# Kernel optimization log

Measured on AMD Instinct MI355X. Metric: run time of the kernel, lower is better.

## Reference

```python
import jax, jax.numpy as jnp
import numpy as np

N = 4096    # nodes per graph
C = 128     # in_channels == out_channels
HEAD = 1
E = 65536   # edges per graph (avg degree 16)


def setup_inputs() -> dict:
    key = jax.random.key(0)
    ks = jax.random.split(key, 24)
    def w(k, shape):
        return jax.random.normal(k, shape, dtype=jnp.float32) * 0.05
    return {
        "x1": jax.random.normal(ks[0], (N, C), dtype=jnp.float32),
        "x2": jax.random.normal(ks[1], (N, C), dtype=jnp.float32),
        "edge_index1": jax.random.randint(ks[2], (2, E), 0, N),
        "edge_index2": jax.random.randint(ks[3], (2, E), 0, N),
        "wl1_w": w(ks[4], (HEAD * C, C)), "wl1_b": w(ks[5], (HEAD * C,)),
        "wr1_w": w(ks[6], (HEAD * C, C)), "wr1_b": w(ks[7], (HEAD * C,)),
        "al1": w(ks[8], (HEAD, C)), "ar1": w(ks[9], (HEAD, C)),
        "wl2_w": w(ks[10], (HEAD * C, C)), "wl2_b": w(ks[11], (HEAD * C,)),
        "wr2_w": w(ks[12], (HEAD * C, C)), "wr2_b": w(ks[13], (HEAD * C,)),
        "al2": w(ks[14], (HEAD, C)), "ar2": w(ks[15], (HEAD, C)),
        "w1_w": w(ks[16], (C, 2 * C)), "w1_b": w(ks[17], (C,)),
        "w2_w": w(ks[18], (C, 2 * C)), "w2_b": w(ks[19], (C,)),
        "lin_w": w(ks[20], (HEAD * C, C)), "lin_b": w(ks[21], (HEAD * C,)),
    }


def _leaky_relu(x):
    return jnp.where(x > 0, x, 0.2 * x)


def _attention(src, tgt, wl, bl, wr, br, al, ar):
    # alpha_l: (N_src,), alpha_r: (N_tot,) -> dense (N_src, N_tot) softmax
    a_l = ((src @ wl.T + bl).reshape(-1, HEAD, C) * al[None]).sum(-1).mean(1)
    a_r = ((tgt @ wr.T + br).reshape(-1, HEAD, C) * ar[None]).sum(-1).mean(1)
    return jax.nn.softmax(_leaky_relu(a_l[:, None] + a_r[None, :]), axis=1)


def _aggr_update(x_i, tgt_all, ei, wl, bl, wr, br, al, ar, ww, wb):
    att = _attention(x_i, tgt_all, wl, bl, wr, br, al, ar)   # (N_i, N_tot)
    ot = x_i - att @ tgt_all                                  # (N_i, C)
    feat = jnp.concatenate([x_i, ot], axis=1)                 # (N_i, 2C)
    n = x_i.shape[0]
    loops = jnp.arange(n)                                     # add_self_loops
    src = jnp.concatenate([ei[0], loops])
    dst = jnp.concatenate([ei[1], loops])
    sums = jax.ops.segment_sum(feat[dst], src, num_segments=n)
    cnt = jax.ops.segment_sum(jnp.ones((src.shape[0],), feat.dtype), src, num_segments=n)
    aggr = sums / cnt[:, None]                                # scatter 'mean'
    return jax.nn.relu(aggr) @ ww.T + wb


def reference(x1, x2, edge_index1, edge_index2,
              wl1_w, wl1_b, wr1_w, wr1_b, al1, ar1,
              wl2_w, wl2_b, wr2_w, wr2_b, al2, ar2,
              w1_w, w1_b, w2_w, w2_b, lin_w, lin_b):
    Xs = [x1, x2]
    eis = [edge_index1, edge_index2]
    layers = [(wl1_w, wl1_b, wr1_w, wr1_b, al1, ar1, w1_w, w1_b),
              (wl2_w, wl2_b, wr2_w, wr2_b, al2, ar2, w2_w, w2_b)]
    for (wl, bl, wr, br, al, ar, ww, wb) in layers:
        tgt = jnp.concatenate(Xs, axis=0)
        Xs = [_aggr_update(Xs[i], tgt, eis[i], wl, bl, wr, br, al, ar, ww, wb)
              for i in range(2)]
    feats = jnp.concatenate(Xs, axis=0) @ lin_w.T + lin_b     # (2N, C)
    return jax.nn.sigmoid(feats @ feats.T)                    # (2N, 2N)
```

## Files before the change

kernel.cpp:

```cpp
#include <hip/hip_runtime.h>
#include <hip/hip_bf16.h>

#define NT 8192
#define NN 4096
#define CD 128
#define NE 65536

typedef __attribute__((ext_vector_type(8))) short bf16x8;
typedef __attribute__((ext_vector_type(16))) float f32x16;
typedef __attribute__((ext_vector_type(4))) float f32x4;

__global__ __launch_bounds__(256) void k_prep(
    const float* __restrict__ x1, const float* __restrict__ x2, float* __restrict__ X,
    const float* __restrict__ W1, const float* __restrict__ W2, const float* __restrict__ WL,
    float* __restrict__ WT1, float* __restrict__ WT2, float* __restrict__ WTL,
    const float* __restrict__ wlw0, const float* __restrict__ wlb0,
    const float* __restrict__ wrw0, const float* __restrict__ wrb0,
    const float* __restrict__ al0, const float* __restrict__ ar0,
    const float* __restrict__ wlw1, const float* __restrict__ wlb1,
    const float* __restrict__ wrw1, const float* __restrict__ wrb1,
    const float* __restrict__ al1, const float* __restrict__ ar1,
    float* __restrict__ VP, int* __restrict__ DEG) {
  int b = blockIdx.x, tid = threadIdx.x;
  int gid = b * 256 + tid;
  {
    const f32x4* s1 = (const f32x4*)x1;
    const f32x4* s2 = (const f32x4*)x2;
    f32x4* d = (f32x4*)X;
    d[gid] = s1[gid];
    d[gid + NN * CD / 4] = s2[gid];
  }
  if (gid < 81920) {
    int idx = gid;
    if (idx < 32768) { int c = idx >> 8, k = idx & 255; WT1[k * 128 + c] = W1[idx]; }
    else if (idx < 65536) { int j = idx - 32768; int c = j >> 8, k = j & 255; WT2[k * 128 + c] = W2[j]; }
    else { int j = idx - 65536; int c = j >> 7, k = j & 127; WTL[k * 128 + c] = WL[j]; }
  }
  if ((b == 508 || b == 509) && tid < 128) {
    int L = b - 508;
    const float* wlw = L ? wlw1 : wlw0;
    const float* wlb = L ? wlb1 : wlb0;
    const float* wrw = L ? wrw1 : wrw0;
    const float* wrb = L ? wrb1 : wrb0;
    const float* alv = L ? al1 : al0;
    const float* arv = L ? ar1 : ar0;
    float* vp = VP + L * 258;
    int c = tid;
    float sl = 0.f, sr = 0.f;
    for (int h = 0; h < 128; ++h) {
      sl += wlw[h * 128 + c] * alv[h];
      sr += wrw[h * 128 + c] * arv[h];
    }
    vp[c] = sl;
    vp[128 + c] = sr;
    if (c < 2) {
      const float* bb = c ? wrb : wlb;
      const float* aa = c ? arv : alv;
      float s = 0.f;
      for (int h = 0; h < 128; ++h) s += bb[h] * aa[h];
      vp[256 + c] = s;
    }
  }
  if (gid < 2 * NN) DEG[gid] = 0;
}

__device__ inline void alar_row(const float* __restrict__ X, const float* __restrict__ VP,
                                float* __restrict__ AL, float* __restrict__ AR,
                                int row, int lane) {
  float x0 = X[row * 128 + lane], x1 = X[row * 128 + 64 + lane];
  float sl = x0 * VP[lane] + x1 * VP[64 + lane];
  float sr = x0 * VP[128 + lane] + x1 * VP[192 + lane];
  #pragma unroll
  for (int m = 1; m < 64; m <<= 1) {
    sl += __shfl_xor(sl, m, 64);
    sr += __shfl_xor(sr, m, 64);
  }
  if (lane == 0) { AL[row] = sl + VP[256]; AR[row] = sr + VP[257]; }
}

__device__ void rank_body(int rb, int tid, const float* __restrict__ AR,
                          int* __restrict__ RANK) {
  __shared__ float tile[1024];
  int jb = rb & 31, tb = rb >> 5;
  int base = tb * 1024;
  for (int t = tid; t < 1024; t += 256) tile[t] = AR[base + t];
  __syncthreads();
  int j = jb * 256 + tid;
  float aj = AR[j];
  int cnt = 0;
  #pragma unroll 8
  for (int u = 0; u < 1024; ++u) {
    float a2 = tile[u];
    cnt += (a2 < aj || (a2 == aj && (base + u) < j)) ? 1 : 0;
  }
  atomicAdd(&RANK[j], cnt);
}

__device__ void scanoff_body(int g, int tid, const int* __restrict__ DEG,
                             int* __restrict__ OFFS, int* __restrict__ CURS) {
  __shared__ int part[256];
  int loc[16];
  int s = 0;
  #pragma unroll
  for (int i = 0; i < 16; ++i) { loc[i] = s; s += DEG[g * NN + tid * 16 + i]; }
  part[tid] = s;
  __syncthreads();
  for (int d = 1; d < 256; d <<= 1) {
    int v = part[tid];
    int o = (tid >= d) ? part[tid - d] : 0;
    __syncthreads();
    part[tid] = v + o;
    __syncthreads();
  }
  int excl = tid ? part[tid - 1] : 0;
  #pragma unroll
  for (int i = 0; i < 16; ++i) {
    int o = excl + loc[i];
    OFFS[g * (NN + 1) + tid * 16 + i] = o;
    CURS[g * NN + tid * 16 + i] = o;
  }
  if (tid == 255) OFFS[g * (NN + 1) + NN] = part[255];
}

__global__ __launch_bounds__(256) void k_s2(
    const int* __restrict__ EI1, const int* __restrict__ EI2, int* __restrict__ DEG,
    const float* __restrict__ X, const float* __restrict__ VP0,
    float* __restrict__ AL, float* __restrict__ AR, int* __restrict__ RANK) {
  int b = blockIdx.x, tid = threadIdx.x;
  if (b < 512) {
    int gid = b * 256 + tid;
    int g = gid >> 16, e = gid & 65535;
    const int* src = g ? EI2 : EI1;
    atomicAdd(&DEG[g * NN + src[e]], 1);
  } else {
    int bb = b - 512;
    if (bb < 32) RANK[bb * 256 + tid] = 0;
    alar_row(X, VP0, AL, AR, bb * 4 + (tid >> 6), tid & 63);
  }
}

__global__ __launch_bounds__(256) void k_s3(
    const int* __restrict__ DEG, int* __restrict__ OFFS, int* __restrict__ CURS,
    const float* __restrict__ AR, int* __restrict__ RANK) {
  int b = blockIdx.x, tid = threadIdx.x;
  if (b < 2) scanoff_body(b, tid, DEG, OFFS, CURS);
  else rank_body(b - 2, tid, AR, RANK);
}

__global__ __launch_bounds__(256) void k_s4(
    const int* __restrict__ EI1, const int* __restrict__ EI2,
    int* __restrict__ CURS, int* __restrict__ ADJ,
    const int* __restrict__ RANK, const float* __restrict__ AR,
    int* __restrict__ PERM, float* __restrict__ ARS) {
  int b = blockIdx.x, tid = threadIdx.x;
  if (b < 512) {
    int gid = b * 256 + tid;
    int g = gid >> 16, e = gid & 65535;
    const int* ei = g ? EI2 : EI1;
    int s = ei[e], d = ei[NE + e];
    int pos = atomicAdd(&CURS[g * NN + s], 1);
    ADJ[g * NE + pos] = d;
  } else {
    int j = (b - 512) * 256 + tid;
    int r = RANK[j];
    PERM[r] = j;
    ARS[r] = AR[j];
  }
}

__global__ void k_rank(const float* __restrict__ AR, int* __restrict__ RANK) {
  rank_body(blockIdx.x, threadIdx.x, AR, RANK);
}
__global__ void k_perm(const int* __restrict__ RANK, const float* __restrict__ AR,
                       int* __restrict__ PERM, float* __restrict__ ARS) {
  int j = blockIdx.x * 256 + threadIdx.x;
  int r = RANK[j];
  PERM[r] = j;
  ARS[r] = AR[j];
}

__global__ __launch_bounds__(256) void k_scanA(
    const float* __restrict__ X, const int* __restrict__ PERM,
    const float* __restrict__ ARS, int* __restrict__ RANK,
    float* __restrict__ P1, float* __restrict__ P2,
    float* __restrict__ CT1, float* __restrict__ CT2,
    float* __restrict__ Q1L, float* __restrict__ Q2L,
    float* __restrict__ QCT1, float* __restrict__ QCT2) {
  __shared__ int pc[64];
  __shared__ float w[2][64];
  __shared__ float part[2][4][32];
  __shared__ float qpart[2][4];
  int b = blockIdx.x;
  if (b < 32) RANK[b * 256 + threadIdx.x] = 0;
  int chunk = b >> 2, sub = b & 3;
  int tid = threadIdx.x;
  int a = tid >> 7;
  int g = (tid >> 5) & 3;
  int cl = tid & 31;
  int c = sub * 32 + cl;
  if (tid < 64) {
    int r = chunk * 64 + tid;
    pc[tid] = PERM[r];
    float ar = ARS[r];
    w[0][tid] = __expf(ar);
    w[1][tid] = __expf(0.2f * ar);
  }
  __syncthreads();
  int t0 = g * 16;
  float loc[16];
  float acc = 0.f;
  #pragma unroll 4
  for (int t = 0; t < 16; ++t) {
    acc += w[a][t0 + t] * X[pc[t0 + t] * 128 + c];
    loc[t] = acc;
  }
  part[a][g][cl] = acc;
  float qloc[16];
  float qacc = 0.f;
  bool doQ = (sub == 0 && cl == 0);
  if (doQ) {
    for (int t = 0; t < 16; ++t) { qacc += w[a][t0 + t]; qloc[t] = qacc; }
    qpart[a][g] = qacc;
  }
  __syncthreads();
  float off = (g > 0 ? part[a][0][cl] : 0.f) + (g > 1 ? part[a][1][cl] : 0.f) +
              (g > 2 ? part[a][2][cl] : 0.f);
  float* P = a ? P2 : P1;
  #pragma unroll 4
  for (int t = 0; t < 16; ++t) P[(chunk * 64 + t0 + t) * 128 + c] = loc[t] + off;
  if (g == 3) (a ? CT2 : CT1)[chunk * 128 + c] = off + acc;
  if (doQ) {
    float qoff = (g > 0 ? qpart[a][0] : 0.f) + (g > 1 ? qpart[a][1] : 0.f) +
                 (g > 2 ? qpart[a][2] : 0.f);
    float* Q = a ? Q2L : Q1L;
    for (int t = 0; t < 16; ++t) Q[chunk * 64 + t0 + t] = qloc[t] + qoff;
    if (g == 3) (a ? QCT2 : QCT1)[chunk] = qoff + qacc;
  }
}

__global__ __launch_bounds__(320) void k_scanB(
    const float* __restrict__ CT1, const float* __restrict__ CT2,
    const float* __restrict__ QCT1, const float* __restrict__ QCT2,
    float* __restrict__ OFF1, float* __restrict__ OFF2,
    float* __restrict__ QOF1, float* __restrict__ QOF2) {
  int tid = threadIdx.x;
  if (tid < 128) {
    float acc = 0.f;
    #pragma unroll 8
    for (int ch = 0; ch < 128; ++ch) { acc += CT1[ch * 128 + tid]; OFF1[ch * 128 + tid] = acc; }
  } else if (tid < 256) {
    int c = tid - 128;
    float acc = 0.f;
    #pragma unroll 8
    for (int ch = 0; ch < 128; ++ch) { acc += CT2[ch * 128 + c]; OFF2[ch * 128 + c] = acc; }
  } else if (tid == 256) {
    float acc = 0.f;
    for (int ch = 0; ch < 128; ++ch) { acc += QCT1[ch]; QOF1[ch] = acc; }
  } else if (tid == 257) {
    float acc = 0.f;
    for (int ch = 0; ch < 128; ++ch) { acc += QCT2[ch]; QOF2[ch] = acc; }
  }
}

__global__ void k_combine(const float* __restrict__ X, const float* __restrict__ AL,
                          const float* __restrict__ ARS,
                          const float* __restrict__ P1, const float* __restrict__ P2,
                          const float* __restrict__ OFF1, const float* __restrict__ OFF2,
                          const float* __restrict__ Q1L, const float* __restrict__ Q2L,
                          const float* __restrict__ QOF1, const float* __restrict__ QOF2,
                          float* __restrict__ OT) {
  int row = blockIdx.x * 2 + (threadIdx.x >> 7);
  int c = threadIdx.x & 127;
  float ali = AL[row];
  float A1 = __expf(ali), A2 = __expf(0.2f * ali);
  float xv = -ali;
  int lo = 0, hi = NT;
  while (lo < hi) {
    int mid = (lo + hi) >> 1;
    if (ARS[mid] <= xv) lo = mid + 1; else hi = mid;
  }
  int b = lo - 1;
  float p1 = 0.f, p2 = 0.f, q1 = 0.f, q2 = 0.f;
  if (b >= 0) {
    int ch = b >> 6;
    p1 = P1[b * 128 + c] + (ch ? OFF1[(ch - 1) * 128 + c] : 0.f);
    p2 = P2[b * 128 + c] + (ch ? OFF2[(ch - 1) * 128 + c] : 0.f);
    q1 = Q1L[b] + (ch ? QOF1[ch - 1] : 0.f);
    q2 = Q2L[b] + (ch ? QOF2[ch - 1] : 0.f);
  }
  float T1 = OFF1[127 * 128 + c];
  float QT1 = QOF1[127];
  float num = A1 * (T1 - p1) + A2 * p2;
  float den = A1 * (QT1 - q1) + A2 * q2;
  OT[row * 128 + c] = X[row * 128 + c] - num / den;
}

__global__ __launch_bounds__(256) void k_aggr(const float* __restrict__ X,
                                              const float* __restrict__ OT,
                                              const int* __restrict__ OFFS,
                                              const int* __restrict__ ADJ,
                                              float* __restrict__ AGGR) {
  int node = blockIdx.x * 4 + (threadIdx.x >> 6);
  int lane = threadIdx.x & 63;
  int g = node >> 12, n = node & (NN - 1);
  const int* off = OFFS + g * (NN + 1);
  const int* adj = ADJ + g * NE;
  int beg = off[n], end = off[n + 1];
  const f32x4* src = (const f32x4*)((lane < 32 ? X : OT) + (size_t)g * NN * CD);
  int c4 = lane & 31;
  f32x4 acc = src[n * 32 + c4];
  for (int e = beg; e < end; ++e) {
    int d = adj[e];
    acc += src[d * 32 + c4];
  }
  f32x4 r = acc / (float)(end - beg + 1);
  ((f32x4*)AGGR)[(size_t)node * 64 + (lane < 32 ? c4 : 32 + c4)] = r;
}

__global__ __launch_bounds__(128) void k_gemmA(const float* __restrict__ A,
                                               const float* __restrict__ WT,
                                               const float* __restrict__ bias,
                                               float* __restrict__ XN,
                                               const float* __restrict__ VP1,
                                               float* __restrict__ AL,
                                               float* __restrict__ AR) {
  __shared__ float sA[8 * 256];
  __shared__ float sB[8 * 128];
  int c = threadIdx.x;
  int r0 = blockIdx.x * 8;
  for (int i = c; i < 8 * 256; i += 128) sA[i] = fmaxf(A[(size_t)r0 * 256 + i], 0.f);
  __syncthreads();
  float acc[8];
  float bc = bias[c];
  #pragma unroll
  for (int i = 0; i < 8; ++i) acc[i] = bc;
  for (int k = 0; k < 256; ++k) {
    float wv = WT[k * 128 + c];
    #pragma unroll
    for (int i = 0; i < 8; ++i) acc[i] += sA[i * 256 + k] * wv;
  }
  #pragma unroll
  for (int i = 0; i < 8; ++i) {
    XN[(r0 + i) * 128 + c] = acc[i];
    sB[i * 128 + c] = acc[i];
  }
  __syncthreads();
  int lane = threadIdx.x & 63, wv_ = threadIdx.x >> 6;
  #pragma unroll
  for (int i = 0; i < 4; ++i) {
    int row = wv_ * 4 + i;
    float x0 = sB[row * 128 + lane], x1 = sB[row * 128 + 64 + lane];
    float sl = x0 * VP1[lane] + x1 * VP1[64 + lane];
    float sr = x0 * VP1[128 + lane] + x1 * VP1[192 + lane];
    #pragma unroll
    for (int m = 1; m < 64; m <<= 1) {
      sl += __shfl_xor(sl, m, 64);
      sr += __shfl_xor(sr, m, 64);
    }
    if (lane == 0) { AL[r0 + row] = sl + VP1[256]; AR[r0 + row] = sr + VP1[257]; }
  }
}

__global__ __launch_bounds__(128) void k_gemmB(const float* __restrict__ A,
                                               const float* __restrict__ WT,
                                               const float* __restrict__ bias,
                                               const float* __restrict__ WTL,
                                               const float* __restrict__ LINB,
                                               __hip_bfloat16* __restrict__ FBF) {
  __shared__ float sA[8 * 256];
  __shared__ float sB[8 * 128];
  int c = threadIdx.x;
  int r0 = blockIdx.x * 8;
  for (int i = c; i < 8 * 256; i += 128) sA[i] = fmaxf(A[(size_t)r0 * 256 + i], 0.f);
  __syncthreads();
  float acc[8];
  float bc = bias[c];
  #pragma unroll
  for (int i = 0; i < 8; ++i) acc[i] = bc;
  for (int k = 0; k < 256; ++k) {
    float wv = WT[k * 128 + c];
    #pragma unroll
    for (int i = 0; i < 8; ++i) acc[i] += sA[i * 256 + k] * wv;
  }
  #pragma unroll
  for (int i = 0; i < 8; ++i) sB[i * 128 + c] = acc[i];
  __syncthreads();
  float acl[8];
  float lb = LINB[c];
  #pragma unroll
  for (int i = 0; i < 8; ++i) acl[i] = lb;
  for (int k = 0; k < 128; ++k) {
    float wl = WTL[k * 128 + c];
    #pragma unroll
    for (int i = 0; i < 8; ++i) acl[i] += sB[i * 128 + k] * wl;
  }
  #pragma unroll
  for (int i = 0; i < 8; ++i) FBF[(r0 + i) * 128 + c] = __float2bfloat16(acl[i]);
}

__device__ inline f32x16 zero16() {
  f32x16 v;
  #pragma unroll
  for (int i = 0; i < 16; ++i) v[i] = 0.f;
  return v;
}

__device__ inline void store_frag(float* __restrict__ out, const f32x16& a,
                                  int grow0, int gcol) {
  #pragma unroll
  for (int r = 0; r < 16; ++r) {
    int rloc = (r & 3) + 8 * (r >> 2);
    float v = a[r];
    out[(size_t)(grow0 + rloc) * 8192 + gcol] =
        __builtin_amdgcn_rcpf(1.f + __expf(-v));
  }
}

__global__ __launch_bounds__(256) void k_final(const unsigned short* __restrict__ F,
                                               float* __restrict__ out) {
  __shared__ unsigned short AT[128 * 128];
  __shared__ unsigned short BT[128 * 128];
  int cb = blockIdx.x, rb = blockIdx.y;
  int tid = threadIdx.x;
  #pragma unroll
  for (int q = 0; q < 8; ++q) {
    int idx = q * 256 + tid;
    int r = idx >> 4, ck = idx & 15;
    unsigned off = (unsigned)((r * 256 + ck * 16) ^ ((r & 7) << 4));
    uint4 va = *(const uint4*)(F + (size_t)(rb * 128 + r) * 128 + ck * 8);
    *(uint4*)((char*)AT + off) = va;
    uint4 vb = *(const uint4*)(F + (size_t)(cb * 128 + r) * 128 + ck * 8);
    *(uint4*)((char*)BT + off) = vb;
  }
  __syncthreads();
  int lane = tid & 63, w = tid >> 6;
  int wr = w >> 1, wc = w & 1;
  int l31 = lane & 31, kh = lane >> 5;
  int xorm = (l31 & 7) << 4;
  int rowA0 = wr * 64 + l31, rowA1 = rowA0 + 32;
  int rowB0 = wc * 64 + l31, rowB1 = rowB0 + 32;
  f32x16 a00 = zero16(), a01 = zero16(), a10 = zero16(), a11 = zero16();
  #pragma unroll
  for (int ks = 0; ks < 8; ++ks) {
    int kb = ks * 32 + kh * 16;
    bf16x8 av0 = *(const bf16x8*)((const char*)AT + ((rowA0 * 256 + kb) ^ xorm));
    bf16x8 av1 = *(const bf16x8*)((const char*)AT + ((rowA1 * 256 + kb) ^ xorm));
    bf16x8 bv0 = *(const bf16x8*)((const char*)BT + ((rowB0 * 256 + kb) ^ xorm));
    bf16x8 bv1 = *(const bf16x8*)((const char*)BT + ((rowB1 * 256 + kb) ^ xorm));
    a00 = __builtin_amdgcn_mfma_f32_32x32x16_bf16(av0, bv0, a00, 0, 0, 0);
    a01 = __builtin_amdgcn_mfma_f32_32x32x16_bf16(av0, bv1, a01, 0, 0, 0);
    a10 = __builtin_amdgcn_mfma_f32_32x32x16_bf16(av1, bv0, a10, 0, 0, 0);
    a11 = __builtin_amdgcn_mfma_f32_32x32x16_bf16(av1, bv1, a11, 0, 0, 0);
  }
  int grow = rb * 128 + wr * 64 + 4 * kh;
  int gcol = cb * 128 + wc * 64 + l31;
  store_frag(out, a00, grow, gcol);
  store_frag(out, a01, grow, gcol + 32);
  store_frag(out, a10, grow + 32, gcol);
  store_frag(out, a11, grow + 32, gcol + 32);
}

extern "C" void kernel_launch(void* const* d_in, const int* in_sizes, int n_in,
                              void* d_out, int out_size, void* d_ws, size_t ws_size,
                              hipStream_t stream) {
  (void)in_sizes; (void)n_in; (void)out_size; (void)ws_size;
  const float* x1 = (const float*)d_in[0];
  const float* x2 = (const float*)d_in[1];
  const int* ei1 = (const int*)d_in[2];
  const int* ei2 = (const int*)d_in[3];
  const float* wl_w[2] = {(const float*)d_in[4], (const float*)d_in[10]};
  const float* wl_b[2] = {(const float*)d_in[5], (const float*)d_in[11]};
  const float* wr_w[2] = {(const float*)d_in[6], (const float*)d_in[12]};
  const float* wr_b[2] = {(const float*)d_in[7], (const float*)d_in[13]};
  const float* alv[2] = {(const float*)d_in[8], (const float*)d_in[14]};
  const float* arv[2] = {(const float*)d_in[9], (const float*)d_in[15]};
  const float* ww_w[2] = {(const float*)d_in[16], (const float*)d_in[18]};
  const float* ww_b[2] = {(const float*)d_in[17], (const float*)d_in[19]};
  const float* lin_w = (const float*)d_in[20];
  const float* lin_b = (const float*)d_in[21];

  char* wp = (char*)d_ws;
  auto alloc = [&](size_t b) -> char* {
    char* p = wp;
    wp += (b + 255) & ~(size_t)255;
    return p;
  };
  float* XA = (float*)alloc((size_t)NT * CD * 4);
  float* XB = (float*)alloc((size_t)NT * CD * 4);
  float* OT = (float*)alloc((size_t)NT * CD * 4);
  float* P1 = (float*)alloc((size_t)NT * CD * 4);
  float* P2 = (float*)alloc((size_t)NT * CD * 4);
  float* AGGR = P1;
  float* CT1 = (float*)alloc(128 * 128 * 4);
  float* CT2 = (float*)alloc(128 * 128 * 4);
  float* OFF1 = (float*)alloc(128 * 128 * 4);
  float* OFF2 = (float*)alloc(128 * 128 * 4);
  float* AL = (float*)alloc(NT * 4);
  float* AR_ = (float*)alloc(NT * 4);
  float* ARS = (float*)alloc(NT * 4);
  float* Q1L = (float*)alloc(NT * 4);
  float* Q2L = (float*)alloc(NT * 4);
  float* QCT1 = (float*)alloc(128 * 4);
  float* QCT2 = (float*)alloc(128 * 4);
  float* QOF1 = (float*)alloc(128 * 4);
  float* QOF2 = (float*)alloc(128 * 4);
  float* VP = (float*)alloc(2 * 258 * 4);
  float* WT1 = (float*)alloc(256 * 128 * 4);
  float* WT2 = (float*)alloc(256 * 128 * 4);
  float* WTL = (float*)alloc(128 * 128 * 4);
  int* RANK = (int*)alloc(NT * 4);
  int* PERM = (int*)alloc(NT * 4);
  int* DEG = (int*)alloc(2 * NN * 4);
  int* OFFS = (int*)alloc(2 * (NN + 1) * 4);
  int* CURS = (int*)alloc(2 * NN * 4);
  int* ADJ = (int*)alloc(2 * NE * 4);
  __hip_bfloat16* FBF = (__hip_bfloat16*)OT;

  k_prep<<<512, 256, 0, stream>>>(x1, x2, XA, ww_w[0], ww_w[1], lin_w, WT1, WT2, WTL,
                                  wl_w[0], wl_b[0], wr_w[0], wr_b[0], alv[0], arv[0],
                                  wl_w[1], wl_b[1], wr_w[1], wr_b[1], alv[1], arv[1],
                                  VP, DEG);
  k_s2<<<2560, 256, 0, stream>>>(ei1, ei2, DEG, XA, VP, AL, AR_, RANK);
  k_s3<<<258, 256, 0, stream>>>(DEG, OFFS, CURS, AR_, RANK);
  k_s4<<<544, 256, 0, stream>>>(ei1, ei2, CURS, ADJ, RANK, AR_, PERM, ARS);
  k_scanA<<<512, 256, 0, stream>>>(XA, PERM, ARS, RANK, P1, P2, CT1, CT2, Q1L, Q2L, QCT1, QCT2);
  k_scanB<<<1, 320, 0, stream>>>(CT1, CT2, QCT1, QCT2, OFF1, OFF2, QOF1, QOF2);
  k_combine<<<4096, 256, 0, stream>>>(XA, AL, ARS, P1, P2, OFF1, OFF2, Q1L, Q2L, QOF1, QOF2, OT);
  k_aggr<<<2048, 256, 0, stream>>>(XA, OT, OFFS, ADJ, AGGR);
  k_gemmA<<<1024, 128, 0, stream>>>(AGGR, WT1, ww_b[0], XB, VP + 258, AL, AR_);
  k_rank<<<256, 256, 0, stream>>>(AR_, RANK);
  k_perm<<<32, 256, 0, stream>>>(RANK, AR_, PERM, ARS);
  k_scanA<<<512, 256, 0, stream>>>(XB, PERM, ARS, RANK, P1, P2, CT1, CT2, Q1L, Q2L, QCT1, QCT2);
  k_scanB<<<1, 320, 0, stream>>>(CT1, CT2, QCT1, QCT2, OFF1, OFF2, QOF1, QOF2);
  k_combine<<<4096, 256, 0, stream>>>(XB, AL, ARS, P1, P2, OFF1, OFF2, Q1L, Q2L, QOF1, QOF2, OT);
  k_aggr<<<2048, 256, 0, stream>>>(XB, OT, OFFS, ADJ, AGGR);
  k_gemmB<<<1024, 128, 0, stream>>>(AGGR, WT2, ww_b[1], WTL, lin_b, FBF);
  k_final<<<dim3(64, 64), 256, 0, stream>>>((const unsigned short*)FBF, (float*)d_out);
}
```

Baseline: 301.2 us.

## Fuse neighbor aggregation into update GEMM and stage final sigmoid output through LDS

Merges the mean-aggregation kernel with the following dense update GEMM, so the aggregated rows go straight into shared memory and are never written to or re-read from global memory. Each wave now gathers two nodes at once, interleaving their neighbor loads. The final sigmoid(F·Fᵀ) kernel writes its MFMA results into LDS and then emits coalesced 16-byte row stores instead of scattered per-element stores. FBF gets its own buffer, which adds a little workspace. The gather loop becomes divergent when the two nodes' degrees differ, and the fused kernel does the GEMM with fewer rows per thread.

Result: no change. 299.0 us (-0.7%).

```diff
diff --git a/kernel.cpp b/kernel.cpp
--- a/kernel.cpp
+++ b/kernel.cpp
@@ -295,107 +295,105 @@
   OT[row * 128 + c] = X[row * 128 + c] - num / den;
 }
 
-__global__ __launch_bounds__(256) void k_aggr(const float* __restrict__ X,
-                                              const float* __restrict__ OT,
-                                              const int* __restrict__ OFFS,
-                                              const int* __restrict__ ADJ,
-                                              float* __restrict__ AGGR) {
-  int node = blockIdx.x * 4 + (threadIdx.x >> 6);
-  int lane = threadIdx.x & 63;
-  int g = node >> 12, n = node & (NN - 1);
-  const int* off = OFFS + g * (NN + 1);
-  const int* adj = ADJ + g * NE;
-  int beg = off[n], end = off[n + 1];
-  const f32x4* src = (const f32x4*)((lane < 32 ? X : OT) + (size_t)g * NN * CD);
-  int c4 = lane & 31;
-  f32x4 acc = src[n * 32 + c4];
-  for (int e = beg; e < end; ++e) {
-    int d = adj[e];
-    acc += src[d * 32 + c4];
-  }
-  f32x4 r = acc / (float)(end - beg + 1);
-  ((f32x4*)AGGR)[(size_t)node * 64 + (lane < 32 ? c4 : 32 + c4)] = r;
-}
-
-__global__ __launch_bounds__(128) void k_gemmA(const float* __restrict__ A,
-                                               const float* __restrict__ WT,
-                                               const float* __restrict__ bias,
-                                               float* __restrict__ XN,
-                                               const float* __restrict__ VP1,
-                                               float* __restrict__ AL,
-                                               float* __restrict__ AR) {
+__global__ __launch_bounds__(256) void k_ag(
+    const float* __restrict__ X, const float* __restrict__ OT,
+    const int* __restrict__ OFFS, const int* __restrict__ ADJ,
+    const float* __restrict__ WT, const float* __restrict__ WB, float* __restrict__ XN,
+    int mode,
+    const float* __restrict__ VP1, float* __restrict__ AL, float* __restrict__ AR,
+    const float* __restrict__ WTL, const float* __restrict__ LINB,
+    __hip_bfloat16* __restrict__ FBF) {
   __shared__ float sA[8 * 256];
   __shared__ float sB[8 * 128];
-  int c = threadIdx.x;
-  int r0 = blockIdx.x * 8;
-  for (int i = c; i < 8 * 256; i += 128) sA[i] = fmaxf(A[(size_t)r0 * 256 + i], 0.f);
-  __syncthreads();
-  float acc[8];
-  float bc = bias[c];
-  #pragma unroll
-  for (int i = 0; i < 8; ++i) acc[i] = bc;
-  for (int k = 0; k < 256; ++k) {
-    float wv = WT[k * 128 + c];
+  int b = blockIdx.x, tid = threadIdx.x;
+  int lane = tid & 63, wv = tid >> 6, c4 = lane & 31;
+  {
+    int beg[2], end[2];
+    const f32x4* srcp[2];
+    const int* adjp[2];
+    f32x4 acc[2];
     #pragma unroll
-    for (int i = 0; i < 8; ++i) acc[i] += sA[i * 256 + k] * wv;
-  }
-  #pragma unroll
-  for (int i = 0; i < 8; ++i) {
-    XN[(r0 + i) * 128 + c] = acc[i];
-    sB[i * 128 + c] = acc[i];
-  }
-  __syncthreads();
-  int lane = threadIdx.x & 63, wv_ = threadIdx.x >> 6;
+    for (int k = 0; k < 2; ++k) {
+      int node = b * 8 + wv * 2 + k;
+      int g = node >> 12, n = node & (NN - 1);
+      beg[k] = OFFS[g * (NN + 1) + n];
+      end[k] = OFFS[g * (NN + 1) + n + 1];
+      srcp[k] = (const f32x4*)((lane < 32 ? X : OT) + (size_t)g * NN * CD);
+      adjp[k] = ADJ + g * NE;
+      acc[k] = srcp[k][n * 32 + c4];
+    }
+    int maxd = max(end[0] - beg[0], end[1] - beg[1]);
+    for (int s = 0; s < maxd; ++s) {
+      #pragma unroll
+      for (int k = 0; k < 2; ++k) {
+        if (beg[k] + s < end[k]) acc[k] += srcp[k][adjp[k][beg[k] + s] * 32 + c4];
+      }
+    }
+    #pragma unroll
+    for (int k = 0; k < 2; ++k) {
+      f32x4 r = acc[k] / (float)(end[k] - beg[k] + 1);
+      #pragma unroll
+      for (int q = 0; q < 4; ++q) r[q] = fmaxf(r[q], 0.f);
+      *(f32x4*)&sA[(wv * 2 + k) * 256 + (lane < 32 ? c4 * 4 : 128 + c4 * 4)] = r;
+    }
+  }
+  __syncthreads();
+  int c = tid & 127, half = tid >> 7;
+  float accv[4];
+  float bc = WB[c];
+  #pragma unroll
+  for (int i = 0; i < 4; ++i) accv[i] = bc;
+  for (int k4 = 0; k4 < 64; ++k4) {
+    float w0 = WT[(k4 * 4 + 0) * 128 + c];
+    float w1v = WT[(k4 * 4 + 1) * 128 + c];
+    float w2v = WT[(k4 * 4 + 2) * 128 + c];
+    float w3 = WT[(k4 * 4 + 3) * 128 + c];
+    #pragma unroll
+    for (int i = 0; i < 4; ++i) {
+      f32x4 av = *(const f32x4*)&sA[(half * 4 + i) * 256 + k4 * 4];
+      accv[i] += av[0] * w0 + av[1] * w1v + av[2] * w2v + av[3] * w3;
+    }
+  }
   #pragma unroll
   for (int i = 0; i < 4; ++i) {
-    int row = wv_ * 4 + i;
-    float x0 = sB[row * 128 + lane], x1 = sB[row * 128 + 64 + lane];
-    float sl = x0 * VP1[lane] + x1 * VP1[64 + lane];
-    float sr = x0 * VP1[128 + lane] + x1 * VP1[192 + lane];
+    sB[(half * 4 + i) * 128 + c] = accv[i];
+    if (mode == 0) XN[(size_t)(b * 8 + half * 4 + i) * 128 + c] = accv[i];
+  }
+  __syncthreads();
+  if (mode == 0) {
     #pragma unroll
-    for (int m = 1; m < 64; m <<= 1) {
-      sl += __shfl_xor(sl, m, 64);
-      sr += __shfl_xor(sr, m, 64);
-    }
-    if (lane == 0) { AL[r0 + row] = sl + VP1[256]; AR[r0 + row] = sr + VP1[257]; }
-  }
-}
-
-__global__ __launch_bounds__(128) void k_gemmB(const float* __restrict__ A,
-                                               const float* __restrict__ WT,
-                                               const float* __restrict__ bias,
-                                               const float* __restrict__ WTL,
-                                               const float* __restrict__ LINB,
-                                               __hip_bfloat16* __restrict__ FBF) {
-  __shared__ float sA[8 * 256];
-  __shared__ float sB[8 * 128];
-  int c = threadIdx.x;
-  int r0 = blockIdx.x * 8;
-  for (int i = c; i < 8 * 256; i += 128) sA[i] = fmaxf(A[(size_t)r0 * 256 + i], 0.f);
-  __syncthreads();
-  float acc[8];
-  float bc = bias[c];
-  #pragma unroll
-  for (int i = 0; i < 8; ++i) acc[i] = bc;
-  for (int k = 0; k < 256; ++k) {
-    float wv = WT[k * 128 + c];
+    for (int k = 0; k < 2; ++k) {
+      int lr = wv * 2 + k;
+      float x0 = sB[lr * 128 + lane], x1 = sB[lr * 128 + 64 + lane];
+      float sl = x0 * VP1[lane] + x1 * VP1[64 + lane];
+      float sr = x0 * VP1[128 + lane] + x1 * VP1[192 + lane];
+      #pragma unroll
+      for (int m = 1; m < 64; m <<= 1) {
+        sl += __shfl_xor(sl, m, 64);
+        sr += __shfl_xor(sr, m, 64);
+      }
+      if (lane == 0) { AL[b * 8 + lr] = sl + VP1[256]; AR[b * 8 + lr] = sr + VP1[257]; }
+    }
+  } else {
+    float acl[4];
+    float lb = LINB[c];
     #pragma unroll
-    for (int i = 0; i < 8; ++i) acc[i] += sA[i * 256 + k] * wv;
-  }
-  #pragma unroll
-  for (int i = 0; i < 8; ++i) sB[i * 128 + c] = acc[i];
-  __syncthreads();
-  float acl[8];
-  float lb = LINB[c];
-  #pragma unroll
-  for (int i = 0; i < 8; ++i) acl[i] = lb;
-  for (int k = 0; k < 128; ++k) {
-    float wl = WTL[k * 128 + c];
+    for (int i = 0; i < 4; ++i) acl[i] = lb;
+    for (int k4 = 0; k4 < 32; ++k4) {
+      float w0 = WTL[(k4 * 4 + 0) * 128 + c];
+      float w1v = WTL[(k4 * 4 + 1) * 128 + c];
+      float w2v = WTL[(k4 * 4 + 2) * 128 + c];
+      float w3 = WTL[(k4 * 4 + 3) * 128 + c];
+      #pragma unroll
+      for (int i = 0; i < 4; ++i) {
+        f32x4 av = *(const f32x4*)&sB[(half * 4 + i) * 128 + k4 * 4];
+        acl[i] += av[0] * w0 + av[1] * w1v + av[2] * w2v + av[3] * w3;
+      }
+    }
     #pragma unroll
-    for (int i = 0; i < 8; ++i) acl[i] += sB[i * 128 + k] * wl;
-  }
-  #pragma unroll
-  for (int i = 0; i < 8; ++i) FBF[(r0 + i) * 128 + c] = __float2bfloat16(acl[i]);
+    for (int i = 0; i < 4; ++i)
+      FBF[(size_t)(b * 8 + half * 4 + i) * 128 + c] = __float2bfloat16(acl[i]);
+  }
 }
 
 __device__ inline f32x16 zero16() {
@@ -405,21 +403,15 @@
   return v;
 }
 
-__device__ inline void store_frag(float* __restrict__ out, const f32x16& a,
-                                  int grow0, int gcol) {
-  #pragma unroll
-  for (int r = 0; r < 16; ++r) {
-    int rloc = (r & 3) + 8 * (r >> 2);
-    float v = a[r];
-    out[(size_t)(grow0 + rloc) * 8192 + gcol] =
-        __builtin_amdgcn_rcpf(1.f + __expf(-v));
-  }
+__device__ inline float sigf(float v) {
+  return __builtin_amdgcn_rcpf(1.f + __expf(-v));
 }
 
 __global__ __launch_bounds__(256) void k_final(const unsigned short* __restrict__ F,
                                                float* __restrict__ out) {
-  __shared__ unsigned short AT[128 * 128];
-  __shared__ unsigned short BT[128 * 128];
+  __shared__ __align__(16) char smem[65536];
+  unsigned short* AT = (unsigned short*)smem;
+  unsigned short* BT = AT + 16384;
   int cb = blockIdx.x, rb = blockIdx.y;
   int tid = threadIdx.x;
   #pragma unroll
@@ -452,12 +444,24 @@
     a10 = __builtin_amdgcn_mfma_f32_32x32x16_bf16(av1, bv0, a10, 0, 0, 0);
     a11 = __builtin_amdgcn_mfma_f32_32x32x16_bf16(av1, bv1, a11, 0, 0, 0);
   }
-  int grow = rb * 128 + wr * 64 + 4 * kh;
-  int gcol = cb * 128 + wc * 64 + l31;
-  store_frag(out, a00, grow, gcol);
-  store_frag(out, a01, grow, gcol + 32);
-  store_frag(out, a10, grow + 32, gcol);
-  store_frag(out, a11, grow + 32, gcol + 32);
+  __syncthreads();
+  float* lw = (float*)smem + w * 4096;
+  #pragma unroll
+  for (int r = 0; r < 16; ++r) {
+    int rl = (r & 3) + 8 * (r >> 2) + 4 * kh;
+    lw[rl * 64 + l31] = sigf(a00[r]);
+    lw[rl * 64 + l31 + 32] = sigf(a01[r]);
+    lw[(rl + 32) * 64 + l31] = sigf(a10[r]);
+    lw[(rl + 32) * 64 + l31 + 32] = sigf(a11[r]);
+  }
+  int grb = rb * 128 + wr * 64, gcb = cb * 128 + wc * 64;
+  #pragma unroll
+  for (int j = 0; j < 16; ++j) {
+    int row = j * 4 + (lane >> 4);
+    int c4 = (lane & 15) * 4;
+    f32x4 v = *(const f32x4*)&lw[row * 64 + c4];
+    *(f32x4*)&out[(size_t)(grb + row) * 8192 + gcb + c4] = v;
+  }
 }
 
 extern "C" void kernel_launch(void* const* d_in, const int* in_sizes, int n_in,
@@ -490,7 +494,7 @@
   float* OT = (float*)alloc((size_t)NT * CD * 4);
   float* P1 = (float*)alloc((size_t)NT * CD * 4);
   float* P2 = (float*)alloc((size_t)NT * CD * 4);
-  float* AGGR = P1;
+  __hip_bfloat16* FBF = (__hip_bfloat16*)alloc((size_t)NT * CD * 2);
   float* CT1 = (float*)alloc(128 * 128 * 4);
   float* CT2 = (float*)alloc(128 * 128 * 4);
   float* OFF1 = (float*)alloc(128 * 128 * 4);
@@ -514,7 +518,6 @@
   int* OFFS = (int*)alloc(2 * (NN + 1) * 4);
   int* CURS = (int*)alloc(2 * NN * 4);
   int* ADJ = (int*)alloc(2 * NE * 4);
-  __hip_bfloat16* FBF = (__hip_bfloat16*)OT;
 
   k_prep<<<512, 256, 0, stream>>>(x1, x2, XA, ww_w[0], ww_w[1], lin_w, WT1, WT2, WTL,
                                   wl_w[0], wl_b[0], wr_w[0], wr_b[0], alv[0], arv[0],
@@ -526,14 +529,14 @@
   k_scanA<<<512, 256, 0, stream>>>(XA, PERM, ARS, RANK, P1, P2, CT1, CT2, Q1L, Q2L, QCT1, QCT2);
   k_scanB<<<1, 320, 0, stream>>>(CT1, CT2, QCT1, QCT2, OFF1, OFF2, QOF1, QOF2);
   k_combine<<<4096, 256, 0, stream>>>(XA, AL, ARS, P1, P2, OFF1, OFF2, Q1L, Q2L, QOF1, QOF2, OT);
-  k_aggr<<<2048, 256, 0, stream>>>(XA, OT, OFFS, ADJ, AGGR);
-  k_gemmA<<<1024, 128, 0, stream>>>(AGGR, WT1, ww_b[0], XB, VP + 258, AL, AR_);
+  k_ag<<<1024, 256, 0, stream>>>(XA, OT, OFFS, ADJ, WT1, ww_b[0], XB,
+                                 0, VP + 258, AL, AR_, WTL, lin_b, FBF);
   k_rank<<<256, 256, 0, stream>>>(AR_, RANK);
   k_perm<<<32, 256, 0, stream>>>(RANK, AR_, PERM, ARS);
   k_scanA<<<512, 256, 0, stream>>>(XB, PERM, ARS, RANK, P1, P2, CT1, CT2, Q1L, Q2L, QCT1, QCT2);
   k_scanB<<<1, 320, 0, stream>>>(CT1, CT2, QCT1, QCT2, OFF1, OFF2, QOF1, QOF2);
   k_combine<<<4096, 256, 0, stream>>>(XB, AL, ARS, P1, P2, OFF1, OFF2, Q1L, Q2L, QOF1, QOF2, OT);
-  k_aggr<<<2048, 256, 0, stream>>>(XB, OT, OFFS, ADJ, AGGR);
-  k_gemmB<<<1024, 128, 0, stream>>>(AGGR, WT2, ww_b[1], WTL, lin_b, FBF);
+  k_ag<<<1024, 256, 0, stream>>>(XB, OT, OFFS, ADJ, WT2, ww_b[1], XB,
+                                 1, VP, AL, AR_, WTL, lin_b, FBF);
   k_final<<<dim3(64, 64), 256, 0, stream>>>((const unsigned short*)FBF, (float*)d_out);
 }
```
